# Kernel tuning notes

Measured on AMD Instinct MI355X. Metric: run time of the kernel, lower is better.

## Reference

```python
import jax, jax.numpy as jnp
import numpy as np

G = 64          # number of global tokens (first G positions are global)
NUM_HEADS = 16
WINDOW = 512    # attention_window (one-sided w = 256)


def _chunk(x, w):
    # x: [BH, S, D] -> overlapping chunks of size 2w with overlap w
    BH, S, D = x.shape
    f = x.reshape(BH, S // w, w, D)
    return jnp.concatenate([f[:, :-1], f[:, 1:]], axis=2)  # [BH, S//w-1, 2w, D]


def _mask_invalid(x, w):
    # x: [B, S, H, 2w+1]; -inf at out-of-sequence window positions
    B, S, H, W = x.shape
    m = jnp.flip(jnp.tril(jnp.ones((w, w + 1), x.dtype)), axis=0)
    m = jnp.pad(m, ((0, S - w), (0, W - w - 1)))
    m = m + jnp.flip(m, axis=(0, 1))
    return jnp.where((m > 0)[None, :, None, :], -jnp.inf, x)


def _sliding_qk(q, k, w):
    # q, k: [B, S, H, D] -> banded scores [B, S, H, 2w+1]
    B, S, H, D = q.shape
    C = S // w - 1
    qf = q.transpose(0, 2, 1, 3).reshape(B * H, S, D)
    kf = k.transpose(0, 2, 1, 3).reshape(B * H, S, D)
    s = jnp.einsum('bcxd,bcyd->bcxy', _chunk(qf, w), _chunk(kf, w))  # [BH,C,2w,2w]
    diag = jnp.pad(s, ((0, 0), (0, 0), (0, 1), (0, 0))).transpose(0, 1, 3, 2)  # [BH,C,2w,2w+1]
    up = jnp.concatenate([diag[:, :, :w, :w + 1], diag[:, -1:, w:, :w + 1]], axis=1)
    z = jnp.zeros((B * H, 1, w, w), diag.dtype)
    low = jnp.concatenate([z, diag[:, :, -(w + 1):-1, w + 1:]], axis=1)
    first = jnp.concatenate([jnp.roll(diag, shift=(1, w), axis=(2, 3))[:, :, :w, :w], z], axis=1)
    low = jnp.where(jnp.arange(C + 1)[None, :, None, None] < 1, first, low)
    full = jnp.concatenate([low, up], axis=-1).reshape(B, H, S, 2 * w + 1).transpose(0, 2, 1, 3)
    return _mask_invalid(full, w)


def _sliding_pv(probs, v, w):
    # probs: [B, S, H, 2w+1], v: [B, S, H, D] -> [B, S, H, D]
    B, S, H, _ = probs.shape
    D = v.shape[-1]
    nc = S // w
    p = probs.transpose(0, 2, 1, 3).reshape(B * H, nc, w, 2 * w + 1)
    vf = v.transpose(0, 2, 1, 3).reshape(B * H, S, D)
    pv = jnp.pad(vf, ((0, 0), (w, w), (0, 0)), constant_values=-1.0)
    idx = jnp.arange(nc)[:, None] * w + jnp.arange(3 * w)[None, :]
    cv = pv[:, idx]  # [BH, nc, 3w, D]
    # pad-and-diagonalize the banded probs into [w, 3w]
    pd = jnp.pad(p, ((0, 0), (0, 0), (0, 0), (0, w + 1)))
    pd = pd.reshape(B * H, nc, w * (3 * w + 2))[:, :, :-w]
    pd = pd.reshape(B * H, nc, w, 3 * w + 1)[:, :, :, :-1]  # [BH,nc,w,3w]
    out = jnp.einsum('bcwd,bcdh->bcwh', pd, cv)
    return out.reshape(B, H, S, D).transpose(0, 2, 1, 3)


def _forward(hidden_states, attention_mask, Wq, bq, Wk, bk, Wv, bv,
             Wqg, bqg, Wkg, bkg, Wvg, bvg, is_index_masked, is_index_global_attn):
    B, S, E = hidden_states.shape
    H = NUM_HEADS
    D = E // H
    w = WINDOW // 2
    q = (hidden_states @ Wq + bq) / jnp.sqrt(jnp.float32(D))
    k = hidden_states @ Wk + bk
    v = hidden_states @ Wv + bv
    q4 = q.reshape(B, S, H, D)
    k4 = k.reshape(B, S, H, D)
    v4 = v.reshape(B, S, H, D)
    local = _sliding_qk(q4, k4, w)                         # [B,S,H,2w+1]
    diag_mask = _sliding_qk(jnp.ones_like(attention_mask), attention_mask, w)  # [B,S,1,2w+1]
    local = local + diag_mask
    # global key columns (first G tokens global) prepended to the band
    g_scores = jnp.einsum('bshd,bghd->bshg', q4, k4[:, :G])
    scores = jnp.concatenate([g_scores, local], axis=-1)   # [B,S,H,G+2w+1]
    probs = jax.nn.softmax(scores, axis=-1)
    probs = jnp.where(is_index_masked[:, :, None, None], 0.0, probs)
    out_g = jnp.einsum('bshg,bghd->bshd', probs[..., :G], v4[:, :G])
    out_l = _sliding_pv(probs[..., G:], v4, w)
    attn_output = (out_g + out_l).reshape(B, S, E)
    # global tokens attend to the full sequence with the *_global projections
    qg = ((hidden_states[:, :G] @ Wqg + bqg) / jnp.sqrt(jnp.float32(D))).reshape(B, G, H, D).transpose(0, 2, 1, 3)
    kg = (hidden_states @ Wkg + bkg).reshape(B, S, H, D).transpose(0, 2, 1, 3)
    vg = (hidden_states @ Wvg + bvg).reshape(B, S, H, D).transpose(0, 2, 1, 3)
    gs = jnp.einsum('bhgd,bhsd->bhgs', qg, kg)             # [B,H,G,S]
    gs = jnp.where(is_index_masked[:, None, None, :], -10000.0, gs)
    gp = jax.nn.softmax(gs, axis=-1)
    go = jnp.einsum('bhgs,bhsd->bhgd', gp, vg).transpose(0, 2, 1, 3).reshape(B, G, E)
    attn_output = attn_output.at[:, :G].set(go)            # scatter global rows
    probs = jnp.where(is_index_global_attn[:, :, None, None], 0.0, probs)
    return attn_output, probs, gp


def setup_inputs() -> dict:
    key = jax.random.key(0)
    B, S, E = 2, 4096, 1024
    ks = jax.random.split(key, 8)
    std = 0.02
    d = lambda k: std * jax.random.normal(k, (E, E), jnp.float32)
    zb = jnp.zeros((E,), jnp.float32)
    return {
        'hidden_states': jax.random.normal(ks[0], (B, S, E), jnp.float32),
        'attention_mask': jnp.zeros((B, S, 1, 1), jnp.float32),
        'Wq': d(ks[1]), 'bq': zb, 'Wk': d(ks[2]), 'bk': zb, 'Wv': d(ks[3]), 'bv': zb,
        'Wqg': d(ks[4]), 'bqg': zb, 'Wkg': d(ks[5]), 'bkg': zb, 'Wvg': d(ks[6]), 'bvg': zb,
        'is_index_masked': jnp.zeros((B, S), bool),
        'is_index_global_attn': jnp.broadcast_to(jnp.arange(S)[None, :] < G, (B, S)),
        'is_global_attn': 1,
    }


def reference(hidden_states, attention_mask, Wq, bq, Wk, bk, Wv, bv,
              Wqg, bqg, Wkg, bkg, Wvg, bvg,
              is_index_masked, is_index_global_attn, is_global_attn):
    # is_global_attn is statically 1 (global path always taken)
    return _forward(hidden_states, attention_mask, Wq, bq, Wk, bk, Wv, bv,
                    Wqg, bqg, Wkg, bkg, Wvg, bvg, is_index_masked, is_index_global_attn)
```

## Files before the change

### kernel.cpp

```cpp
#include <hip/hip_runtime.h>
#include <hip/hip_bf16.h>
#include <cstdint>
#include <cstddef>

typedef short s16x8 __attribute__((ext_vector_type(8)));
typedef float f32x4 __attribute__((ext_vector_type(4)));

#define DEV static __device__ __forceinline__

DEV unsigned short f2bf(float x){
  union { float f; unsigned int u; } v; v.f = x;
  unsigned int u = v.u;
  return (unsigned short)((u + 0x7FFFu + ((u >> 16) & 1u)) >> 16);
}
DEV float bf2f(unsigned short b){
  union { unsigned int u; float f; } v; v.u = ((unsigned int)b) << 16;
  return v.f;
}
DEV void ntst(float* p, float v){ __builtin_nontemporal_store(v, p); }

DEV void bar_lgkm(){
  asm volatile("s_waitcnt lgkmcnt(0)" ::: "memory");
  __builtin_amdgcn_s_barrier();
  __builtin_amdgcn_sched_barrier(0);
}

DEV void gld16(unsigned short* lds, const unsigned short* g){
  __builtin_amdgcn_global_load_lds(
      (const __attribute__((address_space(1))) void*)g,
      (__attribute__((address_space(3))) void*)lds, 16, 0, 0);
}

__global__ __launch_bounds__(256) void cast_x(const float* __restrict__ X,
                                              unsigned short* __restrict__ out,
                                              unsigned short* __restrict__ Xg){
  int i = (blockIdx.x*256 + threadIdx.x)*4;
  float4 v = *(const float4*)(X + i);
  ushort4 r;
  r.x = f2bf(v.x); r.y = f2bf(v.y); r.z = f2bf(v.z); r.w = f2bf(v.w);
  *(ushort4*)(out + i) = r;
  int row = i >> 10;
  int s = row & 4095, b = row >> 12;
  if (s < 64)
    *(ushort4*)(Xg + (size_t)(b*64 + s)*1024 + (i & 1023)) = r;
}

__global__ __launch_bounds__(256) void bias_cat_k(
    const float* bq, const float* bk, const float* bv,
    const float* bkg, const float* bvg, const float* bqg,
    float* __restrict__ bc, float* __restrict__ bqg_o){
  int i = blockIdx.x*256 + threadIdx.x;
  if (i < 5120){
    int slot = i >> 10, c = i & 1023;
    const float* s = (slot==0)?bq:(slot==1)?bk:(slot==2)?bv:(slot==3)?bkg:bvg;
    bc[i] = s[c];
  } else {
    bqg_o[i-5120] = bqg[i-5120];
  }
}

struct WSrc { const float* p[6]; };

__global__ __launch_bounds__(256) void wt_transpose(WSrc srcs,
    unsigned short* __restrict__ Wtcat, unsigned short* __restrict__ Wtqg){
  __shared__ float t[64*66];
  int bi = blockIdx.x;
  int widx = bi >> 8;
  int tile = bi & 255;
  int tn = tile & 15, tk = tile >> 4;
  int k0 = tk*64, n0 = tn*64;
  const float* W = srcs.p[widx];
  int tid = threadIdx.x;
  for (int it=0; it<8; ++it){
    int flat = it*256 + tid;
    int r = flat >> 5, ch = flat & 31;
    *(float2*)&t[r*66 + ch*2] = *(const float2*)(W + (size_t)(k0+r)*1024 + n0 + ch*2);
  }
  __syncthreads();
  unsigned short* dst = (widx==3) ? Wtqg
                      : Wtcat + (size_t)((widx<3)?widx:widx-1)*1048576;
  for (int it=0; it<16; ++it){
    int flat = it*256 + tid;
    int i = flat >> 6, j = flat & 63;
    dst[(size_t)(n0+i)*1024 + k0 + j] = f2bf(t[j*66 + i]);
  }
}

__global__ __launch_bounds__(256) void gemm_bt(
    const unsigned short* __restrict__ A, const unsigned short* __restrict__ Bt,
    const float* __restrict__ bias, unsigned short* __restrict__ C,
    int Astr, int Bstr, int Cstr, int scale_cols)
{
  __shared__ unsigned short lA[128*64];
  __shared__ unsigned short lB[128*64];
  int tid = threadIdx.x, lane = tid & 63, wv = tid >> 6;
  int wm = wv >> 1, wn = wv & 1;
  int lane15 = lane & 15, kh = (lane >> 4) << 3;
  int m0 = blockIdx.y*128, n0 = blockIdx.x*128;
  f32x4 acc[4][4];
  for (int i=0;i<4;i++) for (int j=0;j<4;j++) acc[i][j] = (f32x4){0.f,0.f,0.f,0.f};
  for (int k0 = 0; k0 < 1024; k0 += 64){
#pragma unroll
    for (int it = 0; it < 4; ++it){
      int chunk = it*256 + tid;
      int r = chunk >> 3, ch = chunk & 7;
      int co = ((ch ^ (r & 7)) << 3);
      gld16(&lA[chunk*8], A  + (size_t)(m0+r)*Astr + k0 + co);
      gld16(&lB[chunk*8], Bt + (size_t)(n0+r)*Bstr + k0 + co);
    }
    __syncthreads();
#pragma unroll
    for (int ks = 0; ks < 2; ++ks){
      s16x8 af[4], bfr[4];
#pragma unroll
      for (int i=0;i<4;i++){
        int row = wm*64 + i*16 + lane15;
        af[i] = *(const s16x8*)&lA[(row<<6) + ((ks*32 + kh) ^ ((row&7)<<3))];
      }
#pragma unroll
      for (int j=0;j<4;j++){
        int row = wn*64 + j*16 + lane15;
        bfr[j] = *(const s16x8*)&lB[(row<<6) + ((ks*32 + kh) ^ ((row&7)<<3))];
      }
#pragma unroll
      for (int i=0;i<4;i++)
#pragma unroll
        for (int j=0;j<4;j++)
          acc[i][j] = __builtin_amdgcn_mfma_f32_16x16x32_bf16(af[i], bfr[j], acc[i][j], 0,0,0);
    }
    __syncthreads();
  }
  for (int i=0;i<4;i++){
    int mb = m0 + wm*64 + i*16 + ((lane>>4)<<2);
    for (int j=0;j<4;j++){
      int n = n0 + wn*64 + j*16 + lane15;
      float bb = bias[n];
      float sc = (n < scale_cols) ? 0.125f : 1.0f;
#pragma unroll
      for (int r=0;r<4;r++)
        C[(size_t)(mb+r)*Cstr + n] = f2bf((acc[i][j][r] + bb)*sc);
    }
  }
}

__global__ __launch_bounds__(256) void vt_transpose(
    const unsigned short* __restrict__ proj, unsigned short* __restrict__ dst,
    int coloff){
  __shared__ unsigned short t[64*72];
  int bi = blockIdx.x;
  int sc = bi & 63, h = (bi>>6) & 15, b = bi >> 10;
  int s0 = sc*64;
  int tid = threadIdx.x;
  for (int it=0; it<2; ++it){
    int flat = it*256 + tid;
    int r = flat >> 3, ch = flat & 7;
    *(int4*)&t[r*72 + ch*8] =
      *(const int4*)(proj + (size_t)(b*4096+s0+r)*5120 + coloff + h*64 + ch*8);
  }
  __syncthreads();
  for (int it=0; it<2; ++it){
    int flat = it*256 + tid;
    int d = flat & 63, ch = flat >> 6;
    unsigned short tmp[8];
#pragma unroll
    for (int j=0;j<8;j++) tmp[j] = t[(ch*8+j)*72 + d];
    *(int4*)(dst + ((size_t)(b*16+h)*64 + d)*4096 + s0 + ch*8) = *(int4*)tmp;
  }
}

#define SSTR 612
__global__ __launch_bounds__(512) void sliding_attn(
    const unsigned short* __restrict__ proj,
    const unsigned short* __restrict__ vt,
    const float* __restrict__ amask,
    const unsigned char* __restrict__ maskb,
    float* __restrict__ probs,
    float* __restrict__ attn)
{
  __shared__ float sS[16*SSTR];
  __shared__ float srs[16];
  int bi = (blockIdx.x & 7)*1024 + (blockIdx.x >> 3);
  int ti = bi & 255, h = (bi>>8) & 15, b = bi >> 12;
  int t = ti*16;
  int chk = t >> 8;
  int qu = (chk < 15) ? chk*256 : 3584;
  int ql = (chk >= 1) ? chk*256 : 256;
  int tid = threadIdx.x, lane = tid & 63, wv = tid >> 6;
  int lane15 = lane & 15, kh = (lane >> 4) << 3;
  int rbase = (lane>>4)<<2;

  s16x8 aq0 = {}, aq1 = {}, ak0a = {}, ak0b = {}, ak1a = {}, ak1b = {};
  {
    int qrow = t + lane15;
    if (wv == 0){
      const unsigned short* qp = proj + (size_t)(b*4096+qrow)*5120 + h*64 + kh;
      aq0 = *(const s16x8*)qp;  aq1 = *(const s16x8*)(qp + 32);
    }
    if (wv >= 4){
      const unsigned short* kp0 = proj + (size_t)(b*4096+qrow)*5120 + 1024 + h*64 + kh;
      ak0a = *(const s16x8*)kp0; ak0b = *(const s16x8*)(kp0 + 32);
    }
    if (wv <= 3){
      int krow = t - 1 + lane15; if (krow < 0) krow = 0;
      const unsigned short* kp1 = proj + (size_t)(b*4096+krow)*5120 + 1024 + h*64 + kh;
      ak1a = *(const s16x8*)kp1; ak1b = *(const s16x8*)(kp1 + 32);
    }
  }

  {
    int ct0 = wv*5;
#pragma unroll
    for (int j5 = 0; j5 < 5; ++j5){
      int ct = ct0 + j5;
      if (ct < 37){
        int col = ct*16 + lane15;
        int brow, roff;
        if (ct < 4){        brow = col;               roff = 1024; }
        else if (ct < 20){  brow = ql + 1 + col - 64; roff = 0;
                            if (brow > 4095) brow = 4095; }
        else {              brow = qu + col - 320;    roff = 0; }
        const unsigned short* bp = proj + (size_t)(b*4096+brow)*5120 + roff + h*64 + kh;
        s16x8 b0 = *(const s16x8*)bp;
        s16x8 b1 = *(const s16x8*)(bp + 32);
        s16x8 A0 = (ct<4) ? aq0 : (ct<20) ? ak1a : ak0a;
        s16x8 A1 = (ct<4) ? aq1 : (ct<20) ? ak1b : ak0b;
        f32x4 acc = (f32x4){0.f,0.f,0.f,0.f};
        __builtin_amdgcn_s_setprio(1);
        acc = __builtin_amdgcn_mfma_f32_16x16x32_bf16(A0, b0, acc, 0,0,0);
        acc = __builtin_amdgcn_mfma_f32_16x16x32_bf16(A1, b1, acc, 0,0,0);
        __builtin_amdgcn_s_setprio(0);
        if (col <= 576){
          int sk = (ct >= 4);
#pragma unroll
          for (int r=0;r<4;r++){
            int row = rbase + r;
            sS[row*SSTR + col + (sk ? row : 0)] = acc[r];
          }
        }
      }
    }
  }

  int dg = wv & 3, khalf = wv >> 2;
  int dcol = dg*16 + lane15;
  const unsigned short* vtb = vt + ((size_t)(b*16+h)*64 + dcol)*4096;
  int kc0 = khalf*10, kcn = khalf ? 9 : 10;
  s16x8 vB[10];
#pragma unroll
  for (int j = 0; j < 10; ++j){
    if (j < kcn){
      int kk = (kc0 + j)*32 + kh;
      int key = (kk < 64) ? kk : (t - 320 + kk);
      key = key < 0 ? 0 : (key > 4088 ? 4088 : key);
      vB[j] = *(const s16x8*)(vtb + key);
    }
  }

  bar_lgkm();

  {
    int r0 = wv*2;
    float low_add[2], up_add[2];
#pragma unroll
    for (int rr=0;rr<2;rr++){
      int s = t + r0 + rr;
      low_add[rr] = (s >= 1) ? amask[b*4096 + s - 1] : 0.f;
      up_add[rr]  = amask[b*4096 + s];
    }
    float ereg[2][10];
    float sum4[2] = {0.f,0.f};
#pragma unroll
    for (int i=0;i<10;i++){
      int c = lane + i*64;
      bool inr = (c < 577);
      bool isup = (c >= 320), islow = (c >= 64) & !isup;
      int jup = c - 320, jlow = c - 64;
#pragma unroll
      for (int rr=0;rr<2;rr++){
        int r = r0 + rr;
        float e = 0.f;
        if (inr){
          float v = sS[r*SSTR + c + ((c>=64) ? r : 0)];
          int ii = (t + r) & 255;
          if (isup){
            bool valid = !((chk==15) & (jup >= 256 - ii));
            v = valid ? v + up_add[rr] : -1e30f;
          } else if (islow){
            bool valid = !((chk==0) & (jlow < 256 - ii));
            v = valid ? ((jlow==255) ? 0.f : v + low_add[rr]) : -1e30f;
          }
          e = __expf(v);
          ((unsigned short*)&sS[r*SSTR])[c + ((c>=64) ? r : 0)] = f2bf(e);
        }
        ereg[rr][i] = e;
        sum4[rr] += e;
      }
    }
#pragma unroll
    for (int o=32;o;o>>=1){
#pragma unroll
      for (int rr=0;rr<2;rr++) sum4[rr] += __shfl_xor(sum4[rr], o);
    }
#pragma unroll
    for (int rr=0;rr<2;rr++){
      int r = r0 + rr, s = t + r;
      float rs = 1.f / sum4[rr];
      float mz = maskb[b*4096 + s] ? 0.f : 1.f;
      float pz = (s < 64) ? 0.f : mz;
      float* prow = probs + ((size_t)(b*4096+s)*16 + h)*577;
#pragma unroll
      for (int i=0;i<10;i++){
        int c = lane + i*64;
        if (c < 577) ntst(prow + c, ereg[rr][i] * rs * pz);
      }
      if (lane < 31){
        int zc = (lane < r) ? 64 + lane : 577 + lane;
        ((unsigned short*)&sS[r*SSTR])[zc] = 0;
      }
      if (lane == 0) srs[r] = rs * mz;
    }
  }
  bar_lgkm();

  const unsigned short* prow16 = (const unsigned short*)(sS + (size_t)lane15*SSTR);
  f32x4 oacc = (f32x4){0.f,0.f,0.f,0.f};
  __builtin_amdgcn_s_setprio(1);
#pragma unroll
  for (int j = 0; j < 10; ++j){
    if (j < kcn){
      s16x8 ap = *(const s16x8*)(prow16 + (kc0 + j)*32 + kh);
      oacc = __builtin_amdgcn_mfma_f32_16x16x32_bf16(ap, vB[j], oacc, 0,0,0);
    }
  }
  __builtin_amdgcn_s_setprio(0);
  if (khalf == 1){
#pragma unroll
    for (int r=0;r<4;r++){
      int flat = dg*256 + (rbase + r)*16 + lane15;
      sS[(flat>>8)*SSTR + 336 + (flat & 255)] = oacc[r];
    }
  }
  bar_lgkm();
  if (khalf == 0){
#pragma unroll
    for (int r=0;r<4;r++){
      int flat = dg*256 + (rbase + r)*16 + lane15;
      float part = sS[(flat>>8)*SSTR + 336 + (flat & 255)];
      ntst(attn + (size_t)(b*4096 + t + rbase + r)*1024 + h*64 + dcol,
           (oacc[r] + part) * srs[rbase + r]);
    }
  }
}

__global__ __launch_bounds__(256) void gs_a2(
    const unsigned short* __restrict__ qg,
    const unsigned short* __restrict__ proj,
    const unsigned char* __restrict__ maskb,
    float* __restrict__ gp)
{
  __shared__ unsigned short sQ[64*68];
  int bi = blockIdx.x;
  int sc = bi & 15, h = (bi>>4) & 15, b = bi >> 8;
  int tid = threadIdx.x, lane = tid & 63, wv = tid >> 6;
  int lane15 = lane & 15, kh = (lane >> 4) << 3;
#pragma unroll
  for (int it=0; it<2; ++it){
    int flat = it*256 + tid;
    int g = flat >> 3, ch = (flat & 7) << 3;
    *(s16x8*)&sQ[g*68 + ch] = *(const s16x8*)(qg + (size_t)(b*64+g)*1024 + h*64 + ch);
  }
  __syncthreads();
  s16x8 a[4][2];
#pragma unroll
  for (int gt=0; gt<4; ++gt)
#pragma unroll
    for (int ks=0; ks<2; ++ks)
      a[gt][ks] = *(const s16x8*)&sQ[(gt*16+lane15)*68 + ks*32 + kh];
  int s0 = sc*256 + wv*64;
  float* gpb_ = gp + (size_t)(b*16+h)*64*4096;
#pragma unroll
  for (int st=0; st<4; ++st){
    int s = s0 + st*16 + lane15;
    const unsigned short* kp = proj + (size_t)(b*4096+s)*5120 + 3072 + h*64 + kh;
    s16x8 b0 = *(const s16x8*)kp;
    s16x8 b1 = *(const s16x8*)(kp + 32);
    bool msk = maskb[b*4096 + s] != 0;
    f32x4 acc[4];
#pragma unroll
    for (int gt=0; gt<4; ++gt){
      acc[gt] = (f32x4){0.f,0.f,0.f,0.f};
      acc[gt] = __builtin_amdgcn_mfma_f32_16x16x32_bf16(a[gt][0], b0, acc[gt], 0,0,0);
      acc[gt] = __builtin_amdgcn_mfma_f32_16x16x32_bf16(a[gt][1], b1, acc[gt], 0,0,0);
    }
#pragma unroll
    for (int gt=0; gt<4; ++gt){
#pragma unroll
      for (int r=0;r<4;r++){
        int g = gt*16 + (lane>>4)*4 + r;
        ntst(gpb_ + (size_t)g*4096 + s, msk ? -10000.f : acc[gt][r]);
      }
    }
  }
}

__global__ __launch_bounds__(256) void gs_norm(float* __restrict__ gp,
                                               unsigned short* __restrict__ gpb){
  __shared__ float red[8];
  int bi = blockIdx.x;
  float* row = gp + (size_t)bi*4096;
  int tid = threadIdx.x, lane = tid & 63, wv = tid >> 6;
  float v[16];
  float m = -1e30f;
#pragma unroll
  for (int i=0;i<16;i++){
    v[i] = row[tid + i*256];
    m = fmaxf(m, v[i]);
  }
#pragma unroll
  for (int o=32;o;o>>=1) m = fmaxf(m, __shfl_xor(m, o));
  if (!lane) red[wv] = m;
  __syncthreads();
  m = fmaxf(fmaxf(red[0],red[1]), fmaxf(red[2],red[3]));
  float s = 0.f;
#pragma unroll
  for (int i=0;i<16;i++){
    float e = __expf(v[i] - m);
    v[i] = e;
    s += e;
  }
#pragma unroll
  for (int o=32;o;o>>=1) s += __shfl_xor(s, o);
  if (!lane) red[4+wv] = s;
  __syncthreads();
  s = red[4]+red[5]+red[6]+red[7];
  float rs = 1.f / s;
#pragma unroll
  for (int i=0;i<16;i++){
    float p = v[i] * rs;
    ntst(row + tid + i*256, p);
    gpb[(size_t)bi*4096 + tid + i*256] = f2bf(p);
  }
}

__global__ __launch_bounds__(256) void go_mfma(
    const unsigned short* __restrict__ gpb,
    const unsigned short* __restrict__ vgt,
    float* __restrict__ gop)
{
  int bi = blockIdx.x;
  int kc = bi & 7, bh = bi >> 3;
  int tid = threadIdx.x, lane = tid & 63, wv = tid >> 6;
  int lane15 = lane & 15, kh = (lane >> 4) << 3;
  const unsigned short* arow = gpb + ((size_t)bh*64 + wv*16 + lane15)*4096 + kh;
  const unsigned short* bbase = vgt + (size_t)bh*64*4096 + kh;
  f32x4 acc[4];
#pragma unroll
  for (int j=0;j<4;j++) acc[j] = (f32x4){0.f,0.f,0.f,0.f};
  for (int ks = 0; ks < 16; ++ks){
    int k = kc*512 + ks*32;
    s16x8 a = *(const s16x8*)(arow + k);
#pragma unroll
    for (int j=0;j<4;j++){
      s16x8 bv = *(const s16x8*)(bbase + (size_t)(j*16 + lane15)*4096 + k);
      acc[j] = __builtin_amdgcn_mfma_f32_16x16x32_bf16(a, bv, acc[j], 0,0,0);
    }
  }
  int rq = (lane >> 4) << 2;
  float* o = gop + ((size_t)bh*8 + kc)*4096;
#pragma unroll
  for (int j=0;j<4;j++)
#pragma unroll
    for (int r=0;r<4;r++)
      o[(wv*16 + rq + r)*64 + j*16 + lane15] = acc[j][r];
}

__global__ __launch_bounds__(256) void reduce_go2(
    const float* __restrict__ gop, float* __restrict__ attn){
  int flat = blockIdx.x*256 + threadIdx.x;
  int gd = flat & 4095, bh = flat >> 12;
  int b = bh >> 4, h = bh & 15;
  int g = gd >> 6, d = gd & 63;
  const float* p = gop + (size_t)bh*8*4096 + gd;
  float sum = 0.f;
#pragma unroll
  for (int c=0; c<8; ++c) sum += p[c*4096];
  attn[(size_t)(b*4096 + g)*1024 + h*64 + d] = sum;
}

extern "C" void kernel_launch(void* const* d_in, const int* in_sizes, int n_in,
                              void* d_out, int out_size, void* d_ws, size_t ws_size,
                              hipStream_t stream)
{
  const float* X     = (const float*)d_in[0];
  const float* amask = (const float*)d_in[1];
  const float* Wq  = (const float*)d_in[2];  const float* bq  = (const float*)d_in[3];
  const float* Wk  = (const float*)d_in[4];  const float* bk  = (const float*)d_in[5];
  const float* Wv  = (const float*)d_in[6];  const float* bv  = (const float*)d_in[7];
  const float* Wqg = (const float*)d_in[8];  const float* bqg = (const float*)d_in[9];
  const float* Wkg = (const float*)d_in[10]; const float* bkg = (const float*)d_in[11];
  const float* Wvg = (const float*)d_in[12]; const float* bvg = (const float*)d_in[13];
  const unsigned char* imask = (const unsigned char*)d_in[14];
  (void)in_sizes; (void)n_in; (void)out_size;

  const size_t XBF  = 0;
  const size_t XG   = 16777216;
  const size_t WT   = 17039360;
  const size_t WTQG = 27525120;
  const size_t BC   = 29622272;
  const size_t BQG  = 29642752;
  const size_t PROJ = 29646848;
  const size_t QGO  = 113532928;
  const size_t VT   = 113795072;
  const size_t NEED = 130572288;
  if (ws_size < NEED) return;

  char* ws = (char*)d_ws;
  unsigned short* Xbf   = (unsigned short*)(ws + XBF);
  unsigned short* Xg    = (unsigned short*)(ws + XG);
  unsigned short* Wtcat = (unsigned short*)(ws + WT);
  unsigned short* Wtqg  = (unsigned short*)(ws + WTQG);
  float*          bc    = (float*)(ws + BC);
  float*          bqgo  = (float*)(ws + BQG);
  unsigned short* proj  = (unsigned short*)(ws + PROJ);
  unsigned short* qgo   = (unsigned short*)(ws + QGO);
  unsigned short* vt    = (unsigned short*)(ws + VT);
  unsigned short* gpb   = (unsigned short*)(ws + XBF);
  float*          gop   = (float*)(ws + WT);

  float* attn  = (float*)d_out;
  float* probs = (float*)d_out + 8388608;
  float* gp    = (float*)d_out + 84017152;

  cast_x<<<8192, 256, 0, stream>>>(X, Xbf, Xg);
  bias_cat_k<<<24, 256, 0, stream>>>(bq, bk, bv, bkg, bvg, bqg, bc, bqgo);
  WSrc srcs; srcs.p[0]=Wq; srcs.p[1]=Wk; srcs.p[2]=Wv; srcs.p[3]=Wqg; srcs.p[4]=Wkg; srcs.p[5]=Wvg;
  wt_transpose<<<1536, 256, 0, stream>>>(srcs, Wtcat, Wtqg);
  gemm_bt<<<dim3(40,64), 256, 0, stream>>>(Xbf, Wtcat, bc, proj, 1024, 1024, 5120, 1024);
  gemm_bt<<<dim3(8,1),  256, 0, stream>>>(Xg, Wtqg, bqgo, qgo, 1024, 1024, 1024, 1024);
  vt_transpose<<<2048, 256, 0, stream>>>(proj, vt, 2048);
  sliding_attn<<<8192, 512, 0, stream>>>(proj, vt, amask, imask, probs, attn);
  vt_transpose<<<2048, 256, 0, stream>>>(proj, vt, 4096);
  gs_a2<<<512, 256, 0, stream>>>(qgo, proj, imask, gp);
  gs_norm<<<2048, 256, 0, stream>>>(gp, gpb);
  go_mfma<<<256, 256, 0, stream>>>(gpb, vt, gop);
  reduce_go2<<<512, 256, 0, stream>>>(gop, attn);
}
```

Measured before the change: 375.5 us.

## Replace projection GEMM with 256x256-tile 8-wave kernel using multi-buffered async LDS loads

Adds a new GEMM kernel for the large fused QKV/global projection that uses 256x256 output tiles, 512 threads (8 waves), and a four-slot dynamic LDS ring (128 KB) filled by asynchronous global-to-LDS loads with XOR-swizzled layout. Loads for upcoming k-steps are issued while the current step's MFMAs run. The aim is more data reuse per block and latency hiding for the dominant projection GEMM. The trade-off is fewer blocks (640), which lowers occupancy and may leave CUs underused on tail waves. It also adds a per-call attribute setup for the larger shared memory.

```diff
diff --git a/kernel.cpp b/kernel.cpp
--- a/kernel.cpp
+++ b/kernel.cpp
@@ -83,6 +83,104 @@
     int flat = it*256 + tid;
     int i = flat >> 6, j = flat & 63;
     dst[(size_t)(n0+i)*1024 + k0 + j] = f2bf(t[j*66 + i]);
+  }
+}
+
+#define G8_LDS 131072
+__global__ __launch_bounds__(512) void gemm8(
+    const unsigned short* __restrict__ A, const unsigned short* __restrict__ Bt,
+    const float* __restrict__ bias, unsigned short* __restrict__ C,
+    int Astr, int Bstr, int Cstr, int scale_cols)
+{
+  extern __shared__ unsigned short lds[];
+  int tid = threadIdx.x, lane = tid & 63, wv = tid >> 6;
+  int wr = wv >> 2, wc = wv & 3;
+  int lane15 = lane & 15, kh = (lane >> 4) << 3;
+  int m0 = blockIdx.y*256, n0 = blockIdx.x*256;
+
+  f32x4 acc[8][4];
+#pragma unroll
+  for (int i=0;i<8;i++)
+#pragma unroll
+    for (int j=0;j<4;j++) acc[i][j] = (f32x4){0.f,0.f,0.f,0.f};
+
+#pragma unroll
+  for (int ht=0; ht<4; ++ht){
+    int ktn = ht>>1, half = ht&1;
+    unsigned short* sA = lds + (ht&3)*16384;
+    unsigned short* sB = sA + 8192;
+#pragma unroll
+    for (int cc=0; cc<2; ++cc){
+      int c = cc*512 + tid, r = c>>3, ch = c&7;
+      int co = ktn*64 + ((ch ^ (r&7))<<3);
+      gld16(sA + c*8, A  + (size_t)(m0 + half*128 + r)*Astr + co);
+      gld16(sB + c*8, Bt + (size_t)(n0 + half*128 + r)*Bstr + co);
+    }
+  }
+  asm volatile("s_waitcnt vmcnt(8)" ::: "memory");
+  __builtin_amdgcn_s_barrier();
+  __builtin_amdgcn_sched_barrier(0);
+
+  for (int kt = 0; kt < 16; ++kt){
+    unsigned short* aslot = lds + ((2*kt + wr)&3)*16384;
+    unsigned short* bslot = lds + ((2*kt + (wc>>1))&3)*16384 + 8192;
+    s16x8 bfr[4][2];
+#pragma unroll
+    for (int n=0;n<4;n++){
+      int r = (wc&1)*64 + n*16 + lane15;
+#pragma unroll
+      for (int ks=0;ks<2;ks++)
+        bfr[n][ks] = *(const s16x8*)&bslot[(r<<6) + ((ks*32 + kh) ^ ((r&7)<<3))];
+    }
+    __builtin_amdgcn_s_setprio(1);
+#pragma unroll
+    for (int m=0;m<8;m++){
+      int r = m*16 + lane15;
+      s16x8 a0 = *(const s16x8*)&aslot[(r<<6) + (kh ^ ((r&7)<<3))];
+      s16x8 a1 = *(const s16x8*)&aslot[(r<<6) + ((32 + kh) ^ ((r&7)<<3))];
+#pragma unroll
+      for (int n=0;n<4;n++){
+        acc[m][n] = __builtin_amdgcn_mfma_f32_16x16x32_bf16(a0, bfr[n][0], acc[m][n], 0,0,0);
+        acc[m][n] = __builtin_amdgcn_mfma_f32_16x16x32_bf16(a1, bfr[n][1], acc[m][n], 0,0,0);
+      }
+    }
+    __builtin_amdgcn_s_setprio(0);
+    bar_lgkm();
+    if (kt < 14){
+#pragma unroll
+      for (int hh=0; hh<2; ++hh){
+        int ht = 2*kt + 4 + hh;
+        int ktn = ht>>1, half = ht&1;
+        unsigned short* sA = lds + (ht&3)*16384;
+        unsigned short* sB = sA + 8192;
+#pragma unroll
+        for (int cc=0; cc<2; ++cc){
+          int c = cc*512 + tid, r = c>>3, ch = c&7;
+          int co = ktn*64 + ((ch ^ (r&7))<<3);
+          gld16(sA + c*8, A  + (size_t)(m0 + half*128 + r)*Astr + co);
+          gld16(sB + c*8, Bt + (size_t)(n0 + half*128 + r)*Bstr + co);
+        }
+      }
+      asm volatile("s_waitcnt vmcnt(8)" ::: "memory");
+    } else {
+      asm volatile("s_waitcnt vmcnt(0)" ::: "memory");
+    }
+    __builtin_amdgcn_s_barrier();
+    __builtin_amdgcn_sched_barrier(0);
+  }
+
+#pragma unroll
+  for (int m=0;m<8;m++){
+    int mb = m0 + wr*128 + m*16 + ((lane>>4)<<2);
+#pragma unroll
+    for (int n=0;n<4;n++){
+      int col = n0 + wc*64 + n*16 + lane15;
+      float bb = bias[col];
+      float sc = (col < scale_cols) ? 0.125f : 1.0f;
+#pragma unroll
+      for (int r=0;r<4;r++)
+        C[(size_t)(mb+r)*Cstr + col] = f2bf((acc[m][n][r] + bb)*sc);
+    }
   }
 }
 
@@ -531,12 +629,15 @@
   float* probs = (float*)d_out + 8388608;
   float* gp    = (float*)d_out + 84017152;
 
+  hipFuncSetAttribute((const void*)gemm8,
+                      hipFuncAttributeMaxDynamicSharedMemorySize, G8_LDS);
+
   cast_x<<<8192, 256, 0, stream>>>(X, Xbf, Xg);
   bias_cat_k<<<24, 256, 0, stream>>>(bq, bk, bv, bkg, bvg, bqg, bc, bqgo);
   WSrc srcs; srcs.p[0]=Wq; srcs.p[1]=Wk; srcs.p[2]=Wv; srcs.p[3]=Wqg; srcs.p[4]=Wkg; srcs.p[5]=Wvg;
   wt_transpose<<<1536, 256, 0, stream>>>(srcs, Wtcat, Wtqg);
-  gemm_bt<<<dim3(40,64), 256, 0, stream>>>(Xbf, Wtcat, bc, proj, 1024, 1024, 5120, 1024);
-  gemm_bt<<<dim3(8,1),  256, 0, stream>>>(Xg, Wtqg, bqgo, qgo, 1024, 1024, 1024, 1024);
+  gemm8<<<dim3(20,32), 512, G8_LDS, stream>>>(Xbf, Wtcat, bc, proj, 1024, 1024, 5120, 1024);
+  gemm_bt<<<dim3(8,1), 256, 0, stream>>>(Xg, Wtqg, bqgo, qgo, 1024, 1024, 1024, 1024);
   vt_transpose<<<2048, 256, 0, stream>>>(proj, vt, 2048);
   sliding_attn<<<8192, 512, 0, stream>>>(proj, vt, amask, imask, probs, attn);
   vt_transpose<<<2048, 256, 0, stream>>>(proj, vt, 4096);
```

Measured after the change: 374.0 us (median of 2 runs). Within noise of the previous version (-0.4%).
